# Optimization experiments

Hardware: AMD Instinct MI355X
Metric: run time of the kernel (lower is better)

Reference implementation:

```python
import jax, jax.numpy as jnp
import numpy as np

ITERS = 3
EPS = 1e-6


def setup_inputs() -> dict:
    key = jax.random.key(0)
    k1, k2 = jax.random.split(key, 2)
    a = jax.random.normal(k1, (64, 1152, 1, 1, 1, 1), dtype=jnp.float32)
    v = jax.random.normal(k2, (64, 1152, 32, 4, 4, 1), dtype=jnp.float32)
    logits = jnp.ones((1, 1152, 32, 1, 1, 1), dtype=jnp.float32)
    return {"a": a, "v": v, "logits": logits}


def _squash(s):
    # s: (batch, 1, B, P, P, 1); norm over dim 2 (matches torch code, dim=2)
    norm_sq = jnp.sum(s * s, axis=2, keepdims=True)
    return jnp.sqrt(norm_sq + EPS) / (1.0 + norm_sq) * s


def reference(a, v, logits):
    # a: (batch, A, 1, 1, 1, 1) -- unused (overwritten in original forward)
    # v: (batch, A, B, P, P, 1); logits: (1, A, B, 1, 1, 1)
    batch = v.shape[0]
    b = jnp.broadcast_to(logits, (batch,) + logits.shape[1:])
    p = None
    for i in range(ITERS):
        c = jax.nn.softmax(b, axis=2)                    # route over B
        s = jnp.sum(c * v, axis=1, keepdims=True)        # (batch,1,B,P,P,1)
        p = _squash(s)
        if i < ITERS - 1:
            # agreement: sum over pose dims -> (batch, A, B, 1, 1, 1)
            b = b + jnp.sum(p * v, axis=(-3, -2, -1), keepdims=True)
    p = jnp.squeeze(p, axis=1)                           # (batch, B, P, P, 1)
    a_out = jnp.linalg.norm(p, ord=2, axis=2)            # (batch, B, P, 1)
    return (a_out, p)
```

## Files before the change

kernel.cpp:

```cpp
#include <hip/hip_runtime.h>
#include <math.h>

#define BATCH 64
#define ADIM  1152
#define BDIM  32
#define POSE  16
#define SLICE 512
#define CHUNKS 16
#define ROWS  72
#define RPW   18
#define WAVES 4
#define EPSQ  1e-6f
#define SPART_ITER ((size_t)BATCH * CHUNKS * SLICE)

typedef float v4f __attribute__((ext_vector_type(4)));

__device__ __forceinline__ unsigned pack_bf16x2(float a, float b) {
    unsigned ua = __float_as_uint(a), ub = __float_as_uint(b);
    ua = (ua + 0x7fffu + ((ua >> 16) & 1u)) >> 16;
    ub = (ub + 0x7fffu + ((ub >> 16) & 1u));
    return (ua & 0xffffu) | (ub & 0xffff0000u);
}

__device__ __forceinline__ v4f unpack_bf16x4(uint2 w) {
    v4f r;
    r.x = __uint_as_float(w.x << 16);
    r.y = __uint_as_float(w.x & 0xffff0000u);
    r.z = __uint_as_float(w.y << 16);
    r.w = __uint_as_float(w.y & 0xffff0000u);
    return r;
}


__device__ __forceinline__ void squash_from(const float* sp, int lane,
                                            v4f& sA, v4f& sB, v4f& fac) {
    const v4f* spv = (const v4f*)sp;
    sA = (v4f){0.f, 0.f, 0.f, 0.f};
    sB = (v4f){0.f, 0.f, 0.f, 0.f};
#pragma unroll
    for (int c = 0; c < CHUNKS; ++c) {
        sA += spv[c * 128 + lane];
        sB += spv[c * 128 + 64 + lane];
    }
    v4f nq = sA * sA + sB * sB;
#pragma unroll
    for (int off = 4; off <= 32; off <<= 1) {
        nq.x += __shfl_xor(nq.x, off, 64);
        nq.y += __shfl_xor(nq.y, off, 64);
        nq.z += __shfl_xor(nq.z, off, 64);
        nq.w += __shfl_xor(nq.w, off, 64);
    }
    fac.x = sqrtf(nq.x + EPSQ) / (1.f + nq.x);
    fac.y = sqrtf(nq.y + EPSQ) / (1.f + nq.y);
    fac.z = sqrtf(nq.z + EPSQ) / (1.f + nq.z);
    fac.w = sqrtf(nq.w + EPSQ) / (1.f + nq.w);
}

__device__ __forceinline__ void reduce_write(v4f* red, int lane, int wv,
                                             v4f ra, v4f rb, float* dst) {
    __syncthreads();
    if (wv == 3) { red[lane] = ra; red[64 + lane] = rb; }
    __syncthreads();
    if (wv == 2) { red[lane] += ra; red[64 + lane] += rb; }
    __syncthreads();
    if (wv == 1) { red[lane] += ra; red[64 + lane] += rb; }
    __syncthreads();
    if (wv == 0) {
        v4f* sp = (v4f*)dst;
        sp[lane]      = red[lane] + ra;
        sp[64 + lane] = red[64 + lane] + rb;
    }
}

__global__ __launch_bounds__(256) void route0_compress(
    const float* __restrict__ v,
    const float* __restrict__ logits,
    uint2* __restrict__ tile,
    float* __restrict__ s_part)
{
    const int bt    = blockIdx.x >> 4;
    const int chunk = blockIdx.x & 15;
    const int t     = threadIdx.x;
    const int bc0   = (t >> 2) & 31;
    const int hi    = t >> 7;
    const int a0    = chunk * ROWS;

    __shared__ float w_sh[ROWS * BDIM];
    __shared__ v4f   red[128];

    if (t < ROWS) {
        const float* lr = logits + (size_t)(a0 + t) * BDIM;
        float s = 0.f;
        float e[BDIM];
#pragma unroll
        for (int b = 0; b < BDIM; ++b) { e[b] = __expf(lr[b]); s += e[b]; }
        float rd = 1.f / s;
#pragma unroll
        for (int b = 0; b < BDIM; ++b) w_sh[t * BDIM + b] = e[b] * rd;
    }
    __syncthreads();

    const v4f* vg = (const v4f*)(v + ((size_t)bt * ADIM + a0) * SLICE);
    uint2*     tg = tile + ((size_t)bt * ADIM + a0) * 128;

    v4f acc = (v4f){0.f, 0.f, 0.f, 0.f};
    v4f fA[6], fB[6];
#pragma unroll
    for (int u = 0; u < 6; ++u)
        fA[u] = __builtin_nontemporal_load(&vg[t + 256 * u]);

#pragma unroll
    for (int kk = 0; kk < 6; ++kk) {
        v4f* cur = (kk & 1) ? fB : fA;
        v4f* nxt = (kk & 1) ? fA : fB;
        if (kk + 1 < 6) {
#pragma unroll
            for (int u = 0; u < 6; ++u)
                nxt[u] = __builtin_nontemporal_load(&vg[t + 256 * ((kk + 1) * 6 + u)]);
        }
#pragma unroll
        for (int u = 0; u < 6; ++u) {
            const int k   = kk * 6 + u;
            const int i   = t + 256 * k;
            const int row = 2 * k + hi;
            tg[i] = make_uint2(pack_bf16x2(cur[u].x, cur[u].y),
                               pack_bf16x2(cur[u].z, cur[u].w));
            float c0 = w_sh[row * BDIM + bc0];
            acc += c0 * cur[u];
        }
    }

    __syncthreads();
    if (t >= 128) red[t - 128] = acc;
    __syncthreads();
    if (t < 128) {
        acc += red[t];
        ((v4f*)(s_part + ((size_t)bt * CHUNKS + chunk) * SLICE))[t] = acc;
    }
}

__global__ __launch_bounds__(256) void iter_tile(
    const uint2* __restrict__ tile,
    const float* __restrict__ logits,
    const float* __restrict__ s_part,
    float* __restrict__ s_next,
    int nprev)
{
    const int bt    = blockIdx.x >> 4;
    const int chunk = blockIdx.x & 15;
    const int t     = threadIdx.x;
    const int lane  = t & 63;
    const int wv    = t >> 6;
    const int bq    = lane >> 2;
    const int a0    = chunk * ROWS;
    const int r0    = wv * RPW;

    __shared__ v4f red[128];

    v4f pA = (v4f){0.f, 0.f, 0.f, 0.f};
    v4f pB = (v4f){0.f, 0.f, 0.f, 0.f};
    for (int j = 0; j < nprev; ++j) {
        v4f sA, sB, fac;
        squash_from(s_part + (size_t)j * SPART_ITER +
                    (size_t)bt * CHUNKS * SLICE, lane, sA, sB, fac);
        pA += fac * sA;
        pB += fac * sB;
    }

    const uint2* tb  = tile + ((size_t)bt * ADIM + a0 + r0) * 128;
    const float* lgr = logits + (size_t)(a0 + r0) * BDIM;

    v4f acc0 = (v4f){0.f, 0.f, 0.f, 0.f};
    v4f acc1 = (v4f){0.f, 0.f, 0.f, 0.f};

    uint2 fA[6], fB[6];
#pragma unroll
    for (int u = 0; u < 6; ++u)
        fA[u] = tb[(u >> 1) * 128 + (u & 1) * 64 + lane];

#pragma unroll
    for (int g = 0; g < 6; ++g) {
        uint2* cur = (g & 1) ? fB : fA;
        uint2* nxt = (g & 1) ? fA : fB;
        if (g + 1 < 6) {
#pragma unroll
            for (int u = 0; u < 6; ++u)
                nxt[u] = tb[(3 * (g + 1) + (u >> 1)) * 128 + (u & 1) * 64 + lane];
        }
#pragma unroll
        for (int i = 0; i < 3; ++i) {
            const int rw = 3 * g + i;
            v4f va = unpack_bf16x4(cur[2 * i]);
            v4f vb = unpack_bf16x4(cur[2 * i + 1]);
            float b0 = lgr[rw * BDIM + bq];
            float b1 = lgr[rw * BDIM + 16 + bq];
            float d0 = pA.x * va.x + pA.y * va.y + pA.z * va.z + pA.w * va.w;
            float d1 = pB.x * vb.x + pB.y * vb.y + pB.z * vb.z + pB.w * vb.w;
            d0 += __shfl_xor(d0, 1, 64); d0 += __shfl_xor(d0, 2, 64);
            d1 += __shfl_xor(d1, 1, 64); d1 += __shfl_xor(d1, 2, 64);
            float e0 = __expf(b0 + d0);
            float e1 = __expf(b1 + d1);
            float uu = e0 + e1;
#pragma unroll
            for (int off = 4; off <= 32; off <<= 1)
                uu += __shfl_xor(uu, off, 64);
            float rdc = __builtin_amdgcn_rcpf(uu);
            acc0 += (e0 * rdc) * va;
            acc1 += (e1 * rdc) * vb;
        }
    }

    reduce_write(red, lane, wv, acc0, acc1,
                 s_next + ((size_t)bt * CHUNKS + chunk) * SLICE);
}

__global__ __launch_bounds__(512) void final_out(
    const float* __restrict__ s_part2,
    float* __restrict__ out)
{
    const int bt = blockIdx.x;
    const int t  = threadIdx.x;
    const int pose = t & 15;

    __shared__ float sq[SLICE];
    __shared__ float ns[POSE];

    float sv = 0.f;
#pragma unroll
    for (int c = 0; c < CHUNKS; ++c)
        sv += s_part2[((size_t)bt * CHUNKS + c) * SLICE + t];

    sq[t] = sv * sv;
    __syncthreads();
    if (t < POSE) {
        float a = 0.f;
        for (int b2 = 0; b2 < BDIM; ++b2) a += sq[b2 * POSE + t];
        ns[t] = a;
    }
    __syncthreads();
    float n = ns[pose];
    float pv = sqrtf(n + EPSQ) / (1.f + n) * sv;

    out[8192 + (size_t)bt * SLICE + t] = pv;
    sq[t] = pv * pv;
    __syncthreads();
    if (t < 128) {
        const int b2 = t >> 2, p2 = t & 3;
        float a = 0.f;
#pragma unroll
        for (int p1 = 0; p1 < 4; ++p1) a += sq[b2 * POSE + p1 * 4 + p2];
        out[(size_t)bt * 128 + t] = sqrtf(a);
    }
}

extern "C" void kernel_launch(void* const* d_in, const int* in_sizes, int n_in,
                              void* d_out, int out_size, void* d_ws, size_t ws_size,
                              hipStream_t stream) {
    const float* v      = (const float*)d_in[1];
    const float* logits = (const float*)d_in[2];
    float* out = (float*)d_out;

    uint2* tile   = (uint2*)d_ws;
    float* s_part = (float*)((char*)d_ws + (size_t)BATCH * ADIM * 128 * sizeof(uint2));

    route0_compress<<<dim3(BATCH * CHUNKS), dim3(256), 0, stream>>>(
        v, logits, tile, s_part + 0 * SPART_ITER);
    iter_tile<<<dim3(BATCH * CHUNKS), dim3(256), 0, stream>>>(
        tile, logits, s_part, s_part + 1 * SPART_ITER, 1);
    iter_tile<<<dim3(BATCH * CHUNKS), dim3(256), 0, stream>>>(
        tile, logits, s_part, s_part + 2 * SPART_ITER, 2);
    final_out<<<dim3(BATCH), dim3(512), 0, stream>>>(
        s_part + 2 * SPART_ITER, out);
}
```

Measured before the change: 253.9 us.

## Remap iter_tile lanes to load 16-byte bf16 pairs and stage logits in LDS

Each lane of iter_tile now handles two adjacent pose quads, two per B index, and reads them with one 16-byte uint4 load per row instead of two 8-byte loads. This halves the shuffle stages needed for the agreement dot product and merges the two exps per row into one. Logits for the chunk are staged in shared memory, and the prefetch becomes a triple-buffered schedule of three rows per group. The squash reduction and the final store are remapped to the new interleaved layout, which adds an extra shuffle stage and more registers per lane.

```diff
diff --git a/kernel.cpp b/kernel.cpp
--- a/kernel.cpp
+++ b/kernel.cpp
@@ -9,7 +9,6 @@
 #define CHUNKS 16
 #define ROWS  72
 #define RPW   18
-#define WAVES 4
 #define EPSQ  1e-6f
 #define SPART_ITER ((size_t)BATCH * CHUNKS * SLICE)
 
@@ -22,54 +21,44 @@
     return (ua & 0xffffu) | (ub & 0xffff0000u);
 }
 
-__device__ __forceinline__ v4f unpack_bf16x4(uint2 w) {
+__device__ __forceinline__ v4f unpack_bf16x4(unsigned lo, unsigned hi) {
     v4f r;
-    r.x = __uint_as_float(w.x << 16);
-    r.y = __uint_as_float(w.x & 0xffff0000u);
-    r.z = __uint_as_float(w.y << 16);
-    r.w = __uint_as_float(w.y & 0xffff0000u);
+    r.x = __uint_as_float(lo << 16);
+    r.y = __uint_as_float(lo & 0xffff0000u);
+    r.z = __uint_as_float(hi << 16);
+    r.w = __uint_as_float(hi & 0xffff0000u);
     return r;
 }
 
 
-__device__ __forceinline__ void squash_from(const float* sp, int lane,
-                                            v4f& sA, v4f& sB, v4f& fac) {
+__device__ __forceinline__ void squash_pair(const float* sp, int lane,
+                                            v4f& sA, v4f& sB,
+                                            v4f& facA, v4f& facB) {
     const v4f* spv = (const v4f*)sp;
     sA = (v4f){0.f, 0.f, 0.f, 0.f};
     sB = (v4f){0.f, 0.f, 0.f, 0.f};
 #pragma unroll
     for (int c = 0; c < CHUNKS; ++c) {
-        sA += spv[c * 128 + lane];
-        sB += spv[c * 128 + 64 + lane];
-    }
-    v4f nq = sA * sA + sB * sB;
-#pragma unroll
-    for (int off = 4; off <= 32; off <<= 1) {
-        nq.x += __shfl_xor(nq.x, off, 64);
-        nq.y += __shfl_xor(nq.y, off, 64);
-        nq.z += __shfl_xor(nq.z, off, 64);
-        nq.w += __shfl_xor(nq.w, off, 64);
-    }
-    fac.x = sqrtf(nq.x + EPSQ) / (1.f + nq.x);
-    fac.y = sqrtf(nq.y + EPSQ) / (1.f + nq.y);
-    fac.z = sqrtf(nq.z + EPSQ) / (1.f + nq.z);
-    fac.w = sqrtf(nq.w + EPSQ) / (1.f + nq.w);
-}
-
-__device__ __forceinline__ void reduce_write(v4f* red, int lane, int wv,
-                                             v4f ra, v4f rb, float* dst) {
-    __syncthreads();
-    if (wv == 3) { red[lane] = ra; red[64 + lane] = rb; }
-    __syncthreads();
-    if (wv == 2) { red[lane] += ra; red[64 + lane] += rb; }
-    __syncthreads();
-    if (wv == 1) { red[lane] += ra; red[64 + lane] += rb; }
-    __syncthreads();
-    if (wv == 0) {
-        v4f* sp = (v4f*)dst;
-        sp[lane]      = red[lane] + ra;
-        sp[64 + lane] = red[64 + lane] + rb;
-    }
+        sA += spv[c * 128 + 2 * lane];
+        sB += spv[c * 128 + 2 * lane + 1];
+    }
+    v4f nA = sA * sA;
+    v4f nB = sB * sB;
+#pragma unroll
+    for (int off = 2; off <= 32; off <<= 1) {
+        nA.x += __shfl_xor(nA.x, off, 64); nA.y += __shfl_xor(nA.y, off, 64);
+        nA.z += __shfl_xor(nA.z, off, 64); nA.w += __shfl_xor(nA.w, off, 64);
+        nB.x += __shfl_xor(nB.x, off, 64); nB.y += __shfl_xor(nB.y, off, 64);
+        nB.z += __shfl_xor(nB.z, off, 64); nB.w += __shfl_xor(nB.w, off, 64);
+    }
+    facA.x = sqrtf(nA.x + EPSQ) / (1.f + nA.x);
+    facA.y = sqrtf(nA.y + EPSQ) / (1.f + nA.y);
+    facA.z = sqrtf(nA.z + EPSQ) / (1.f + nA.z);
+    facA.w = sqrtf(nA.w + EPSQ) / (1.f + nA.w);
+    facB.x = sqrtf(nB.x + EPSQ) / (1.f + nB.x);
+    facB.y = sqrtf(nB.y + EPSQ) / (1.f + nB.y);
+    facB.z = sqrtf(nB.z + EPSQ) / (1.f + nB.z);
+    facB.w = sqrtf(nB.w + EPSQ) / (1.f + nB.w);
 }
 
 __global__ __launch_bounds__(256) void route0_compress(
@@ -140,7 +129,7 @@
 }
 
 __global__ __launch_bounds__(256) void iter_tile(
-    const uint2* __restrict__ tile,
+    const uint4* __restrict__ tile,
     const float* __restrict__ logits,
     const float* __restrict__ s_part,
     float* __restrict__ s_next,
@@ -151,67 +140,92 @@
     const int t     = threadIdx.x;
     const int lane  = t & 63;
     const int wv    = t >> 6;
-    const int bq    = lane >> 2;
+    const int bb    = lane >> 1;
     const int a0    = chunk * ROWS;
     const int r0    = wv * RPW;
 
-    __shared__ v4f red[128];
+    __shared__ float lg_sh[ROWS * BDIM];
+    __shared__ v4f   red[128];
+
+    for (int i = t; i < ROWS * BDIM; i += 256)
+        lg_sh[i] = logits[(size_t)a0 * BDIM + i];
+    __syncthreads();
 
     v4f pA = (v4f){0.f, 0.f, 0.f, 0.f};
     v4f pB = (v4f){0.f, 0.f, 0.f, 0.f};
     for (int j = 0; j < nprev; ++j) {
-        v4f sA, sB, fac;
-        squash_from(s_part + (size_t)j * SPART_ITER +
-                    (size_t)bt * CHUNKS * SLICE, lane, sA, sB, fac);
-        pA += fac * sA;
-        pB += fac * sB;
-    }
-
-    const uint2* tb  = tile + ((size_t)bt * ADIM + a0 + r0) * 128;
-    const float* lgr = logits + (size_t)(a0 + r0) * BDIM;
+        v4f sA, sB, fA_, fB_;
+        squash_pair(s_part + (size_t)j * SPART_ITER +
+                    (size_t)bt * CHUNKS * SLICE, lane, sA, sB, fA_, fB_);
+        pA += fA_ * sA;
+        pB += fB_ * sB;
+    }
+
+    const uint4* tb = tile + ((size_t)bt * ADIM + a0 + r0) * 64;
 
     v4f acc0 = (v4f){0.f, 0.f, 0.f, 0.f};
     v4f acc1 = (v4f){0.f, 0.f, 0.f, 0.f};
-
-    uint2 fA[6], fB[6];
-#pragma unroll
-    for (int u = 0; u < 6; ++u)
-        fA[u] = tb[(u >> 1) * 128 + (u & 1) * 64 + lane];
-
-#pragma unroll
-    for (int g = 0; g < 6; ++g) {
-        uint2* cur = (g & 1) ? fB : fA;
-        uint2* nxt = (g & 1) ? fA : fB;
-        if (g + 1 < 6) {
-#pragma unroll
-            for (int u = 0; u < 6; ++u)
-                nxt[u] = tb[(3 * (g + 1) + (u >> 1)) * 128 + (u & 1) * 64 + lane];
-        }
-#pragma unroll
-        for (int i = 0; i < 3; ++i) {
-            const int rw = 3 * g + i;
-            v4f va = unpack_bf16x4(cur[2 * i]);
-            v4f vb = unpack_bf16x4(cur[2 * i + 1]);
-            float b0 = lgr[rw * BDIM + bq];
-            float b1 = lgr[rw * BDIM + 16 + bq];
-            float d0 = pA.x * va.x + pA.y * va.y + pA.z * va.z + pA.w * va.w;
-            float d1 = pB.x * vb.x + pB.y * vb.y + pB.z * vb.z + pB.w * vb.w;
-            d0 += __shfl_xor(d0, 1, 64); d0 += __shfl_xor(d0, 2, 64);
-            d1 += __shfl_xor(d1, 1, 64); d1 += __shfl_xor(d1, 2, 64);
-            float e0 = __expf(b0 + d0);
-            float e1 = __expf(b1 + d1);
-            float uu = e0 + e1;
-#pragma unroll
-            for (int off = 4; off <= 32; off <<= 1)
-                uu += __shfl_xor(uu, off, 64);
-            float rdc = __builtin_amdgcn_rcpf(uu);
-            acc0 += (e0 * rdc) * va;
-            acc1 += (e1 * rdc) * vb;
-        }
-    }
-
-    reduce_write(red, lane, wv, acc0, acc1,
-                 s_next + ((size_t)bt * CHUNKS + chunk) * SLICE);
+    uint4 bufA[3], bufB[3], bufC[3];
+
+#define PREFETCH(DST, G)                                                  \
+    {                                                                     \
+        _Pragma("unroll")                                                 \
+        for (int u = 0; u < 3; ++u)                                       \
+            DST[u] = tb[((G) * 3 + u) * 64 + lane];                       \
+    }
+
+#define COMPUTE(SRC, G)                                                   \
+    {                                                                     \
+        _Pragma("unroll")                                                 \
+        for (int i = 0; i < 3; ++i) {                                     \
+            const int rw = r0 + (G) * 3 + i;                              \
+            v4f va = unpack_bf16x4(SRC[i].x, SRC[i].y);                   \
+            v4f vb = unpack_bf16x4(SRC[i].z, SRC[i].w);                   \
+            float d = pA.x * va.x + pA.y * va.y + pA.z * va.z             \
+                    + pA.w * va.w + pB.x * vb.x + pB.y * vb.y             \
+                    + pB.z * vb.z + pB.w * vb.w;                          \
+            d += __shfl_xor(d, 1, 64);                                    \
+            float e = __expf(lg_sh[rw * BDIM + bb] + d);                  \
+            float uu = e;                                                 \
+            uu += __shfl_xor(uu, 2, 64);                                  \
+            uu += __shfl_xor(uu, 4, 64);                                  \
+            uu += __shfl_xor(uu, 8, 64);                                  \
+            uu += __shfl_xor(uu, 16, 64);                                 \
+            uu += __shfl_xor(uu, 32, 64);                                 \
+            float cc = e * __builtin_amdgcn_rcpf(uu);                     \
+            acc0 += cc * va;                                              \
+            acc1 += cc * vb;                                              \
+        }                                                                 \
+    }
+
+    PREFETCH(bufA, 0)
+    PREFETCH(bufB, 1)
+    PREFETCH(bufC, 2)
+    COMPUTE(bufA, 0)
+    PREFETCH(bufA, 3)
+    COMPUTE(bufB, 1)
+    PREFETCH(bufB, 4)
+    COMPUTE(bufC, 2)
+    PREFETCH(bufC, 5)
+    COMPUTE(bufA, 3)
+    COMPUTE(bufB, 4)
+    COMPUTE(bufC, 5)
+
+#undef PREFETCH
+#undef COMPUTE
+
+    __syncthreads();
+    if (wv == 3) { red[2 * lane] = acc0; red[2 * lane + 1] = acc1; }
+    __syncthreads();
+    if (wv == 2) { red[2 * lane] += acc0; red[2 * lane + 1] += acc1; }
+    __syncthreads();
+    if (wv == 1) { red[2 * lane] += acc0; red[2 * lane + 1] += acc1; }
+    __syncthreads();
+    if (wv == 0) {
+        v4f* sp = (v4f*)(s_next + ((size_t)bt * CHUNKS + chunk) * SLICE);
+        sp[2 * lane]     = red[2 * lane] + acc0;
+        sp[2 * lane + 1] = red[2 * lane + 1] + acc1;
+    }
 }
 
 __global__ __launch_bounds__(512) void final_out(
@@ -266,9 +280,9 @@
     route0_compress<<<dim3(BATCH * CHUNKS), dim3(256), 0, stream>>>(
         v, logits, tile, s_part + 0 * SPART_ITER);
     iter_tile<<<dim3(BATCH * CHUNKS), dim3(256), 0, stream>>>(
-        tile, logits, s_part, s_part + 1 * SPART_ITER, 1);
+        (const uint4*)tile, logits, s_part, s_part + 1 * SPART_ITER, 1);
     iter_tile<<<dim3(BATCH * CHUNKS), dim3(256), 0, stream>>>(
-        tile, logits, s_part, s_part + 2 * SPART_ITER, 2);
+        (const uint4*)tile, logits, s_part, s_part + 2 * SPART_ITER, 2);
     final_out<<<dim3(BATCH), dim3(512), 0, stream>>>(
         s_part + 2 * SPART_ITER, out);
 }
```

Result: slower. 259.5 us (+2.2%).
